# Kernel tuning notes

Hardware: AMD Instinct MI355X
Metric: run time of the kernel (lower is better)

## Reference

```python
import jax, jax.numpy as jnp
import numpy as np

N_QUBITS = 10
T_STEPS = 10
NDATA = 1024
DIM = 2 ** N_QUBITS
PI = float(np.pi)


def setup_inputs() -> dict:
    key = jax.random.key(0)
    k1, k2, k3, k4, k5 = jax.random.split(key, 5)
    # random complex amplitudes (normalized to unit states inside reference)
    inputs_re = jax.random.normal(k1, (NDATA, DIM), dtype=jnp.float32)
    inputs_im = jax.random.normal(k2, (NDATA, DIM), dtype=jnp.float32)
    # diffusion noise schedule diff_hs (t,) in (0,1]
    diff_hs = jax.random.uniform(k5, (T_STEPS,), dtype=jnp.float32, minval=0.1, maxval=1.0)
    # var_1 = diff_hs.repeat(3n) in torch == tile -> index k scaled by diff_hs[k % t]
    var_1 = jnp.tile(diff_hs, 3 * N_QUBITS)                                  # (3*n*t,)
    phis = (jax.random.uniform(k3, (NDATA, 3 * N_QUBITS * T_STEPS), dtype=jnp.float32)
            * (PI / 4.0) - (PI / 8.0)) * var_1[None, :]
    gs = (jax.random.uniform(k4, (NDATA, T_STEPS), dtype=jnp.float32) * 0.2 + 0.4) * diff_hs[None, :]
    return {"inputs_re": inputs_re, "inputs_im": inputs_im, "phis": phis, "gs": gs}


def _apply_1q(psi, M, i):
    """Apply per-sample 2x2 gate M (B,2,2) on qubit i (qubit 0 = MSB) to psi (B, 2**n)."""
    left = 2 ** i
    right = 2 ** (N_QUBITS - 1 - i)
    s = psi.reshape(NDATA, left, 2, right)
    s = jnp.einsum('bxy,bayc->baxc', M, s)
    return s.reshape(NDATA, DIM)


def _scramble(inputs_re, inputs_im, phis, gs):
    n, t = N_QUBITS, T_STEPS
    psi = (inputs_re + 1j * inputs_im).astype(jnp.complex64)
    psi = psi / jnp.linalg.norm(psi, axis=1, keepdims=True)  # unit input states

    # precompute sum_{i<j} z_i z_j per basis state for the diagonal RZZ product
    idx = jnp.arange(DIM)
    bits = (idx[:, None] >> jnp.arange(n - 1, -1, -1)[None, :]) & 1  # (DIM, n), qubit0=MSB
    z = 1.0 - 2.0 * bits.astype(jnp.float32)
    zsum = z.sum(axis=1)
    pairsum = 0.5 * (zsum ** 2 - n)                                   # (DIM,)
    inv = 1.0 / (2.0 * np.sqrt(float(n)))

    for tt in range(t):
        base = 3 * n * tt
        for i in range(n):
            a = phis[:, base + i]            # first RZ angle
            th = phis[:, base + n + i]       # RY angle
            b = phis[:, base + 2 * n + i]    # second RZ angle
            c = jnp.cos(0.5 * th).astype(jnp.complex64)
            s = jnp.sin(0.5 * th).astype(jnp.complex64)
            ea_m = jnp.exp(-0.5j * a); ea_p = jnp.exp(0.5j * a)
            eb_m = jnp.exp(-0.5j * b); eb_p = jnp.exp(0.5j * b)
            # M = RZ(b) @ RY(th) @ RZ(a), per sample (B,2,2)
            M = jnp.stack([
                jnp.stack([eb_m * c * ea_m, -eb_m * s * ea_p], axis=-1),
                jnp.stack([eb_p * s * ea_m,  eb_p * c * ea_p], axis=-1),
            ], axis=-2)
            psi = _apply_1q(psi, M, i)
        # all RZZ(i,j, theta) gates are diagonal with shared theta -> single fused phase
        theta = (gs[:, tt] * inv).astype(jnp.complex64)
        psi = psi * jnp.exp(-0.5j * theta[:, None] * pairsum[None, :])
    return psi


def reference(inputs_re, inputs_im, phis, gs):
    psi = _scramble(inputs_re, inputs_im, phis, gs)
    return jnp.stack([psi.real, psi.imag])  # (2, Ndata, 2**n) float32
```

## Files before the change

kernel.cpp:

```cpp
#include <hip/hip_runtime.h>

#define NQ 10
#define TS 10
#define DIM 1024
#define ND 1024

typedef _Float16 h4 __attribute__((ext_vector_type(4)));
typedef float f4 __attribute__((ext_vector_type(4)));

__device__ __forceinline__ f4 mfma16(h4 a, h4 b, f4 c) {
    return __builtin_amdgcn_mfma_f32_16x16x16f16(a, b, c, 0, 0, 0);
}
__device__ __forceinline__ h4 cvt_h4(f4 x) {
    h4 r;
    r[0] = (_Float16)x[0]; r[1] = (_Float16)x[1];
    r[2] = (_Float16)x[2]; r[3] = (_Float16)x[3];
    return r;
}
__device__ __forceinline__ float hsel(int ob, int ib, float cq, float sq) {
    return (ob == ib) ? cq : (ob ? sq : -sq);
}

__global__ __launch_bounds__(64, 1) void qsim_kernel(
    const float* __restrict__ re_in, const float* __restrict__ im_in,
    const float* __restrict__ phis, const float* __restrict__ gs,
    float* __restrict__ out)
{
    const int sample = blockIdx.x;
    const int lane = threadIdx.x;
    const int quad = lane >> 4;
    const int cc = lane & 15;
    const int c3 = (cc >> 3) & 1, c2 = (cc >> 2) & 1, c1 = (cc >> 1) & 1, c0 = cc & 1;
    const int q1 = quad >> 1, q0 = quad & 1;

    const float* pr_in = re_in + sample * DIM;
    const float* pi_in = im_in + sample * DIM;
    const float* ph = phis + sample * (3 * NQ * TS);
    const float* gsp = gs + sample * TS;

    f4 Sr[4], Si[4];
    const int lbase = 256 * quad + cc;
#pragma unroll
    for (int n = 0; n < 4; ++n)
#pragma unroll
        for (int s = 0; s < 4; ++s) {
            Sr[n][s] = pr_in[lbase + 64 * s + 16 * n];
            Si[n][s] = pi_in[lbase + 64 * s + 16 * n];
        }

    const float inv = 0.15811388300841897f;
    float gk[TS];
#pragma unroll
    for (int t = 0; t < TS; ++t) gk[t] = -0.5f * (gsp[t] * inv);

    float nrm = 0.f;
#pragma unroll
    for (int n = 0; n < 4; ++n)
#pragma unroll
        for (int s = 0; s < 4; ++s) nrm += Sr[n][s] * Sr[n][s] + Si[n][s] * Si[n][s];
#pragma unroll
    for (int off = 32; off >= 1; off >>= 1) nrm += __shfl_xor(nrm, off, 64);
    const float scl = rsqrtf(nrm);
#pragma unroll
    for (int n = 0; n < 4; ++n) { Sr[n] *= scl; Si[n] *= scl; }

    float psv[4][4];
    const int pbase = __popc(quad) + __popc(cc);
#pragma unroll
    for (int n = 0; n < 4; ++n)
#pragma unroll
        for (int s = 0; s < 4; ++s) {
            const int p = pbase + __popc(n) + __popc(s);
            const int z = NQ - 2 * p;
            psv[n][s] = 0.5f * (float)(z * z - NQ);
        }
    const float fq1 = (float)q1, fq0 = (float)q0;
    const float fc3 = (float)c3, fc2 = (float)c2, fc1 = (float)c1, fc0 = (float)c0;

    float bprev[NQ];
#pragma unroll
    for (int i = 0; i < NQ; ++i) bprev[i] = 0.f;
    float kk = 0.f;

    auto apply_diag = [&](const float* v, float kcur) {
        float sv = 0.f;
#pragma unroll
        for (int i = 0; i < NQ; ++i) sv += v[i];
        float base = fmaf(-0.5f, sv, 0.f);
        base = fmaf(fq1, v[0], base); base = fmaf(fq0, v[1], base);
        base = fmaf(fc3, v[6], base); base = fmaf(fc2, v[7], base);
        base = fmaf(fc1, v[8], base); base = fmaf(fc0, v[9], base);
        const float addS[4] = {0.f, v[3], v[2], v[2] + v[3]};
        const float addN[4] = {0.f, v[5], v[4], v[4] + v[5]};
#pragma unroll
        for (int n = 0; n < 4; ++n)
#pragma unroll
            for (int s = 0; s < 4; ++s) {
                const float phi = fmaf(kcur, psv[n][s], base + addN[n] + addS[s]);
                const float sp = __sinf(phi);
                const float cp = __cosf(phi);
                const float xr = Sr[n][s], xi = Si[n][s];
                Sr[n][s] = cp * xr - sp * xi;
                Si[n][s] = sp * xr + cp * xi;
            }
    };

    const f4 zf4 = {0.f, 0.f, 0.f, 0.f};

    for (int tt = 0; tt < TS; ++tt) {
        float phs[30];
#pragma unroll
        for (int j = 0; j < 30; ++j) phs[j] = ph[30 * tt + j];

        float v[NQ];
#pragma unroll
        for (int i = 0; i < NQ; ++i) v[i] = phs[i] + bprev[i];
        apply_diag(v, kk);

        float C[NQ], S[NQ];
#pragma unroll
        for (int g = 0; g < NQ; ++g) {
            const float h = 0.5f * phs[10 + g];
            S[g] = __sinf(h);
            C[g] = __cosf(h);
        }

        h4 gb;
        {
            const float f01 = hsel(c3, q1, C[0], S[0]) * hsel(c2, q0, C[1], S[1]);
#pragma unroll
            for (int s = 0; s < 4; ++s) {
                const float e = f01 * hsel(c1, s >> 1, C[2], S[2])
                                    * hsel(c0, s & 1,  C[3], S[3]);
                gb[s] = (_Float16)e;
            }
        }

        h4 hb[4][4];
        {
            const float F67 = hsel(c3, q1, C[6], S[6]) * hsel(c2, q0, C[7], S[7]);
            float F89[4];
#pragma unroll
            for (int s = 0; s < 4; ++s)
                F89[s] = F67 * hsel(c1, s >> 1, C[8], S[8])
                             * hsel(c0, s & 1,  C[9], S[9]);
#pragma unroll
            for (int n = 0; n < 4; ++n)
#pragma unroll
                for (int j = 0; j < 4; ++j) {
                    const float F45 = hsel(n >> 1, j >> 1, C[4], S[4])
                                    * hsel(n & 1,  j & 1,  C[5], S[5]);
#pragma unroll
                    for (int s = 0; s < 4; ++s)
                        hb[n][j][s] = (_Float16)(F45 * F89[s]);
                }
        }

        h4 ar[4], ai[4];
#pragma unroll
        for (int n = 0; n < 4; ++n) { ar[n] = cvt_h4(Sr[n]); ai[n] = cvt_h4(Si[n]); }
        f4 Tr[4], Ti[4];
#pragma unroll
        for (int n = 0; n < 4; ++n) {
            Tr[n] = mfma16(ar[n], gb, zf4);
            Ti[n] = mfma16(ai[n], gb, zf4);
        }
        h4 tr[4], ti[4];
#pragma unroll
        for (int n = 0; n < 4; ++n) { tr[n] = cvt_h4(Tr[n]); ti[n] = cvt_h4(Ti[n]); }

#pragma unroll
        for (int n = 0; n < 4; ++n) {
            f4 accr = zf4, acci = zf4;
#pragma unroll
            for (int j = 0; j < 4; ++j) {
                accr = mfma16(tr[j], hb[n][j], accr);
                acci = mfma16(ti[j], hb[n][j], acci);
            }
            Sr[n] = accr;
            Si[n] = acci;
        }

#pragma unroll
        for (int i = 0; i < NQ; ++i) bprev[i] = phs[20 + i];
        kk = gk[tt];
    }

    apply_diag(bprev, kk);

    float* outr = out + sample * DIM;
    float* outi = out + ND * DIM + sample * DIM;
#pragma unroll
    for (int n = 0; n < 4; ++n)
#pragma unroll
        for (int s = 0; s < 4; ++s) {
            outr[lbase + 64 * s + 16 * n] = Sr[n][s];
            outi[lbase + 64 * s + 16 * n] = Si[n][s];
        }
}

extern "C" void kernel_launch(void* const* d_in, const int* in_sizes, int n_in,
                              void* d_out, int out_size, void* d_ws, size_t ws_size,
                              hipStream_t stream) {
    const float* re_in = (const float*)d_in[0];
    const float* im_in = (const float*)d_in[1];
    const float* phis  = (const float*)d_in[2];
    const float* gs    = (const float*)d_in[3];
    float* out = (float*)d_out;
    qsim_kernel<<<ND, 64, 0, stream>>>(re_in, im_in, phis, gs, out);
}
```

Measured before the change: 80.10 us.

## Software-pipeline next-step trig and gate tiles behind MFMA chain; use packed fp16 conversion

Restructures the time loop so the diagonal phase trig and the fp16 gate tiles for step t+1 are computed while step t's MFMA chain runs. The idea is to let VALU/transcendental work overlap with the dependent MFMA latency in a single-wave block. It also switches float-to-half conversions to packed cvt_pkrtz (round-toward-zero instead of round-to-nearest). The cost is much higher register pressure from holding double-buffered tiles and trig arrays, plus a small change in rounding behaviour.

Result: no change. 80.02 us (-0.1%).

```diff
diff --git a/kernel.cpp b/kernel.cpp
--- a/kernel.cpp
+++ b/kernel.cpp
@@ -6,15 +6,16 @@
 #define ND 1024
 
 typedef _Float16 h4 __attribute__((ext_vector_type(4)));
+typedef __fp16  p2 __attribute__((ext_vector_type(2)));
 typedef float f4 __attribute__((ext_vector_type(4)));
 
 __device__ __forceinline__ f4 mfma16(h4 a, h4 b, f4 c) {
     return __builtin_amdgcn_mfma_f32_16x16x16f16(a, b, c, 0, 0, 0);
 }
 __device__ __forceinline__ h4 cvt_h4(f4 x) {
-    h4 r;
-    r[0] = (_Float16)x[0]; r[1] = (_Float16)x[1];
-    r[2] = (_Float16)x[2]; r[3] = (_Float16)x[3];
+    p2 lo = __builtin_amdgcn_cvt_pkrtz(x[0], x[1]);
+    p2 hi = __builtin_amdgcn_cvt_pkrtz(x[2], x[3]);
+    h4 r; r[0] = lo[0]; r[1] = lo[1]; r[2] = hi[0]; r[3] = hi[1];
     return r;
 }
 __device__ __forceinline__ float hsel(int ob, int ib, float cq, float sq) {
@@ -77,12 +78,11 @@
     const float fq1 = (float)q1, fq0 = (float)q0;
     const float fc3 = (float)c3, fc2 = (float)c2, fc1 = (float)c1, fc0 = (float)c0;
 
-    float bprev[NQ];
-#pragma unroll
-    for (int i = 0; i < NQ; ++i) bprev[i] = 0.f;
-    float kk = 0.f;
-
-    auto apply_diag = [&](const float* v, float kcur) {
+    float DCP[4][4], DSP[4][4];
+    h4 gb; h4 hb[4][4];
+    float bcur[NQ];
+
+    auto make_trig = [&](const float* v, float kcur, float dcp[4][4], float dsp[4][4]) {
         float sv = 0.f;
 #pragma unroll
         for (int i = 0; i < NQ; ++i) sv += v[i];
@@ -97,63 +97,91 @@
 #pragma unroll
             for (int s = 0; s < 4; ++s) {
                 const float phi = fmaf(kcur, psv[n][s], base + addN[n] + addS[s]);
-                const float sp = __sinf(phi);
-                const float cp = __cosf(phi);
+                dcp[n][s] = __cosf(phi);
+                dsp[n][s] = __sinf(phi);
+            }
+    };
+    auto make_tiles = [&](const float* th_src, h4& gbo, h4 hbo[4][4]) {
+        float C[NQ], S[NQ];
+#pragma unroll
+        for (int g = 0; g < NQ; ++g) {
+            const float h = 0.5f * th_src[g];
+            S[g] = __sinf(h);
+            C[g] = __cosf(h);
+        }
+        {
+            const float f01 = hsel(c3, q1, C[0], S[0]) * hsel(c2, q0, C[1], S[1]);
+            float e[4];
+#pragma unroll
+            for (int s = 0; s < 4; ++s)
+                e[s] = f01 * hsel(c1, s >> 1, C[2], S[2]) * hsel(c0, s & 1, C[3], S[3]);
+            p2 lo = __builtin_amdgcn_cvt_pkrtz(e[0], e[1]);
+            p2 hi = __builtin_amdgcn_cvt_pkrtz(e[2], e[3]);
+            gbo[0] = lo[0]; gbo[1] = lo[1]; gbo[2] = hi[0]; gbo[3] = hi[1];
+        }
+        const float F67 = hsel(c3, q1, C[6], S[6]) * hsel(c2, q0, C[7], S[7]);
+        float F89[4];
+#pragma unroll
+        for (int s = 0; s < 4; ++s)
+            F89[s] = F67 * hsel(c1, s >> 1, C[8], S[8]) * hsel(c0, s & 1, C[9], S[9]);
+#pragma unroll
+        for (int n = 0; n < 4; ++n)
+#pragma unroll
+            for (int j = 0; j < 4; ++j) {
+                const float F45 = hsel(n >> 1, j >> 1, C[4], S[4])
+                                * hsel(n & 1,  j & 1,  C[5], S[5]);
+                p2 lo = __builtin_amdgcn_cvt_pkrtz(F45 * F89[0], F45 * F89[1]);
+                p2 hi = __builtin_amdgcn_cvt_pkrtz(F45 * F89[2], F45 * F89[3]);
+                hbo[n][j][0] = lo[0]; hbo[n][j][1] = lo[1];
+                hbo[n][j][2] = hi[0]; hbo[n][j][3] = hi[1];
+            }
+    };
+
+    {
+        float phs[30];
+#pragma unroll
+        for (int j = 0; j < 30; ++j) phs[j] = ph[j];
+        make_trig(&phs[0], 0.f, DCP, DSP);
+        make_tiles(&phs[10], gb, hb);
+#pragma unroll
+        for (int i = 0; i < NQ; ++i) bcur[i] = phs[20 + i];
+    }
+
+    const f4 zf4 = {0.f, 0.f, 0.f, 0.f};
+
+    for (int tt = 0; tt < TS; ++tt) {
+#pragma unroll
+        for (int n = 0; n < 4; ++n)
+#pragma unroll
+            for (int s = 0; s < 4; ++s) {
+                const float cp = DCP[n][s], sp = DSP[n][s];
                 const float xr = Sr[n][s], xi = Si[n][s];
                 Sr[n][s] = cp * xr - sp * xi;
                 Si[n][s] = sp * xr + cp * xi;
             }
-    };
-
-    const f4 zf4 = {0.f, 0.f, 0.f, 0.f};
-
-    for (int tt = 0; tt < TS; ++tt) {
-        float phs[30];
-#pragma unroll
-        for (int j = 0; j < 30; ++j) phs[j] = ph[30 * tt + j];
-
-        float v[NQ];
-#pragma unroll
-        for (int i = 0; i < NQ; ++i) v[i] = phs[i] + bprev[i];
-        apply_diag(v, kk);
-
-        float C[NQ], S[NQ];
-#pragma unroll
-        for (int g = 0; g < NQ; ++g) {
-            const float h = 0.5f * phs[10 + g];
-            S[g] = __sinf(h);
-            C[g] = __cosf(h);
-        }
-
-        h4 gb;
+
+        h4 gbN; h4 hbN[4][4];
+        float DCPn[4][4], DSPn[4][4];
+        float bnext[NQ];
+        const bool last = (tt == TS - 1);
         {
-            const float f01 = hsel(c3, q1, C[0], S[0]) * hsel(c2, q0, C[1], S[1]);
-#pragma unroll
-            for (int s = 0; s < 4; ++s) {
-                const float e = f01 * hsel(c1, s >> 1, C[2], S[2])
-                                    * hsel(c0, s & 1,  C[3], S[3]);
-                gb[s] = (_Float16)e;
-            }
-        }
-
-        h4 hb[4][4];
-        {
-            const float F67 = hsel(c3, q1, C[6], S[6]) * hsel(c2, q0, C[7], S[7]);
-            float F89[4];
-#pragma unroll
-            for (int s = 0; s < 4; ++s)
-                F89[s] = F67 * hsel(c1, s >> 1, C[8], S[8])
-                             * hsel(c0, s & 1,  C[9], S[9]);
-#pragma unroll
-            for (int n = 0; n < 4; ++n)
-#pragma unroll
-                for (int j = 0; j < 4; ++j) {
-                    const float F45 = hsel(n >> 1, j >> 1, C[4], S[4])
-                                    * hsel(n & 1,  j & 1,  C[5], S[5]);
-#pragma unroll
-                    for (int s = 0; s < 4; ++s)
-                        hb[n][j][s] = (_Float16)(F45 * F89[s]);
-                }
+            float phsN[30];
+            if (!last) {
+#pragma unroll
+                for (int j = 0; j < 30; ++j) phsN[j] = ph[30 * (tt + 1) + j];
+            } else {
+#pragma unroll
+                for (int j = 0; j < 30; ++j) phsN[j] = 0.f;
+            }
+            float vN[NQ];
+#pragma unroll
+            for (int i = 0; i < NQ; ++i) vN[i] = phsN[i] + bcur[i];
+            make_trig(vN, gk[tt], DCPn, DSPn);
+            if (!last) {
+                make_tiles(&phsN[10], gbN, hbN);
+#pragma unroll
+                for (int i = 0; i < NQ; ++i) bnext[i] = phsN[20 + i];
+            }
         }
 
         h4 ar[4], ai[4];
@@ -168,7 +196,6 @@
         h4 tr[4], ti[4];
 #pragma unroll
         for (int n = 0; n < 4; ++n) { tr[n] = cvt_h4(Tr[n]); ti[n] = cvt_h4(Ti[n]); }
-
 #pragma unroll
         for (int n = 0; n < 4; ++n) {
             f4 accr = zf4, acci = zf4;
@@ -182,11 +209,29 @@
         }
 
 #pragma unroll
-        for (int i = 0; i < NQ; ++i) bprev[i] = phs[20 + i];
-        kk = gk[tt];
+        for (int n = 0; n < 4; ++n)
+#pragma unroll
+            for (int s = 0; s < 4; ++s) { DCP[n][s] = DCPn[n][s]; DSP[n][s] = DSPn[n][s]; }
+        if (!last) {
+            gb = gbN;
+#pragma unroll
+            for (int n = 0; n < 4; ++n)
+#pragma unroll
+                for (int j = 0; j < 4; ++j) hb[n][j] = hbN[n][j];
+#pragma unroll
+            for (int i = 0; i < NQ; ++i) bcur[i] = bnext[i];
+        }
     }
 
-    apply_diag(bprev, kk);
+#pragma unroll
+    for (int n = 0; n < 4; ++n)
+#pragma unroll
+        for (int s = 0; s < 4; ++s) {
+            const float cp = DCP[n][s], sp = DSP[n][s];
+            const float xr = Sr[n][s], xi = Si[n][s];
+            Sr[n][s] = cp * xr - sp * xi;
+            Si[n][s] = sp * xr + cp * xi;
+        }
 
     float* outr = out + sample * DIM;
     float* outi = out + ND * DIM + sample * DIM;
```
